# Kernel optimization log

Measured on AMD Instinct MI355X. Metric: run time of the kernel, lower is better.

## Reference

```python
import jax, jax.numpy as jnp
import numpy as np

B, T, N = 256, 4096, 8   # batch, timesteps, n_actions (state channels = 2n)
H = 64                    # hidden width of the t -> latent_x surrogate MLP
P = 2 * N + 2 * N * N     # params dim: g(n) | mu(n) | Pi(n^2) | Gamma(n^2) = 144
DATA_W, PHYS_W, SUP_W = 1.0, 1.0, 1.0


def setup_inputs() -> dict:
    key = jax.random.key(0)
    ks = jax.random.split(key, 10)
    return {
        "t": jax.random.uniform(ks[0], (B, T), dtype=jnp.float32),
        "x_target": jax.random.normal(ks[1], (B, 2 * N, T), dtype=jnp.float32),
        "params_pred": jax.random.normal(ks[2], (B, P), dtype=jnp.float32) * 0.1,
        "params_target": jax.random.normal(ks[3], (B, P), dtype=jnp.float32) * 0.1,
        "ic_pred": jax.random.normal(ks[4], (B, 2 * N), dtype=jnp.float32),
        "ic_target": jax.random.normal(ks[5], (B, 2 * N), dtype=jnp.float32),
        "W1": jax.random.normal(ks[6], (1, H), dtype=jnp.float32) * 0.5,
        "b1": jax.random.normal(ks[7], (H,), dtype=jnp.float32) * 0.1,
        "W2": jax.random.normal(ks[8], (H, 2 * N), dtype=jnp.float32) * 0.2,
        "b2": jax.random.normal(ks[9], (2 * N,), dtype=jnp.float32) * 0.1,
    }


def _observables(latent, mu, n):
    # compute_observables_torch (assumed): obs = [a, relu(q - mu)], smooth=False
    a = latent[..., :n]
    q = latent[..., n:]
    return jnp.concatenate([a, jax.nn.relu(q - mu)], axis=-1)  # (B,T,2n)


def _rhs(state_T, g, mu, Pi, Gamma, n):
    # preference_dynamics_rhs_torch (assumed):
    #   da/dt = g + Pi @ x - a ;  dx/dt = (Gamma @ a) * (mu - x)
    a = state_T[..., :n]            # (B,T,n)
    x = state_T[..., n:]            # (B,T,n)
    da = g + jnp.einsum('bij,btj->bti', Pi, x) - a
    dx = jnp.einsum('bij,btj->bti', Gamma, a) * (mu - x)
    return jnp.concatenate([da, dx], axis=-1)  # (B,T,2n)


def reference(t, x_target, params_pred, params_target, ic_pred, ic_target, W1, b1, W2, b2):
    n = N
    g = params_pred[:, :n]                                    # (B,n)
    mu = params_pred[:, n:2 * n]                              # (B,n)
    Pi = params_pred[:, 2 * n:2 * n + n * n].reshape(B, n, n)
    Gamma = params_pred[:, 2 * n + n * n:].reshape(B, n, n)
    mu_t = mu[:, None, :]                                     # broadcast over T

    def state_fn(tt):
        # surrogate for the upstream net producing latent_x from t (pointwise in t)
        h = jnp.tanh(tt[..., None] @ W1 + b1)   # (B,T,H)
        latent = h @ W2 + b2                    # (B,T,2n)
        return _observables(latent, mu_t, n)    # (B,T,2n)

    # batched d(state)/dt in ONE forward-mode pass (replaces the T-iteration
    # torch.autograd.grad loop); valid because state[b,τ] depends only on t[b,τ].
    state_T, dstate_dt = jax.jvp(state_fn, (t,), (jnp.ones_like(t),))

    state = jnp.transpose(state_T, (0, 2, 1))                 # (B,2n,T)
    data_loss = jnp.mean((state - x_target) ** 2)

    rhs = _rhs(state_T, g[:, None, :], mu_t, Pi, Gamma, n)
    physics_loss = jnp.mean((dstate_dt - rhs) ** 2)

    pred_pi = jnp.concatenate([params_pred, ic_pred], axis=1)
    tgt_pi = jnp.concatenate([params_target, ic_target], axis=1)
    supervised_loss = jnp.mean((pred_pi - tgt_pi) ** 2)

    return DATA_W * data_loss + PHYS_W * physics_loss + SUP_W * supervised_loss
```

## Files before the change

### kernel.cpp

```cpp
#include <hip/hip_runtime.h>
#include <math.h>

#define B_    256
#define T_    4096
#define N_    8
#define TWON_ 16
#define H_    64
#define P_    144
#define BLK   256
#define CHUNKS (T_ / BLK)
#define PSTRIDE 20

#define INV_MAIN  (1.0f / (float)(B_ * TWON_ * T_))
#define INV_SUP   (1.0f / (float)(B_ * (P_ + TWON_)))

#define TWO_LOG2E 2.8853900817779268f

typedef __fp16   half2_t __attribute__((ext_vector_type(2)));
typedef _Float16 half8_t __attribute__((ext_vector_type(8)));
typedef float    f32x4   __attribute__((ext_vector_type(4)));

union HPack { half2_t h2[4]; half8_t h8; };
union RPack { uint4 u4[4]; half2_t h2[16]; };

__device__ __forceinline__ float wave_reduce(float v) {
    #pragma unroll
    for (int off = 32; off > 0; off >>= 1) v += __shfl_down(v, off, 64);
    return v;
}

__global__ __launch_bounds__(BLK)
void pinn_main_kernel(const float* __restrict__ t_in,
                      const float* __restrict__ x_target,
                      const float* __restrict__ params_pred,
                      const float* __restrict__ params_target,
                      const float* __restrict__ ic_pred,
                      const float* __restrict__ ic_target,
                      const float* __restrict__ W1,
                      const float* __restrict__ b1,
                      const float* __restrict__ W2,
                      const float* __restrict__ b2,
                      float* __restrict__ out) {
    __shared__ __align__(16) half2_t spk[BLK * PSTRIDE];
    __shared__ float sg[N_], smu[N_], sPi[N_ * N_], sGam[N_ * N_];
    __shared__ float swsum[BLK / 64];

    const int tid  = threadIdx.x;
    const int b    = blockIdx.y;
    const int lane = tid & 63;
    const int wv   = tid >> 6;
    const int q    = lane >> 4;
    const int mn   = lane & 15;
    const int k0   = q * 8;

    const float* pp = params_pred + b * P_;
    if (tid < N_) { sg[tid] = pp[tid]; smu[tid] = pp[N_ + tid]; }
    if (tid >= 64  && tid < 64 + N_ * N_)  sPi[tid - 64]   = pp[2 * N_ + (tid - 64)];
    if (tid >= 128 && tid < 128 + N_ * N_) sGam[tid - 128] = pp[2 * N_ + N_ * N_ + (tid - 128)];

    float sup = 0.0f;
    if (blockIdx.x == 0) {
        if (tid < P_) {
            const float d = pp[tid] - params_target[b * P_ + tid];
            sup = d * d;
        }
        if (tid < TWON_) {
            const float d = ic_pred[b * TWON_ + tid] - ic_target[b * TWON_ + tid];
            sup = fmaf(d, d, sup);
        }
    }

    float zwlo[8], zblo[8], zwhi[8], zbhi[8];
    HPack Blo, Bhi, Plo, Phi;
    #pragma unroll
    for (int j2 = 0; j2 < 4; ++j2) {
        const int ka = k0 + 2 * j2, kb = ka + 1;
        const float w1a = W1[ka],      w1b = W1[kb];
        const float w1c = W1[32 + ka], w1d = W1[32 + kb];
        zwlo[2*j2] = TWO_LOG2E * w1a; zwlo[2*j2+1] = TWO_LOG2E * w1b;
        zwhi[2*j2] = TWO_LOG2E * w1c; zwhi[2*j2+1] = TWO_LOG2E * w1d;
        zblo[2*j2] = TWO_LOG2E * b1[ka];      zblo[2*j2+1] = TWO_LOG2E * b1[kb];
        zbhi[2*j2] = TWO_LOG2E * b1[32 + ka]; zbhi[2*j2+1] = TWO_LOG2E * b1[32 + kb];
        const float wa = W2[ka * TWON_ + mn],        wb = W2[kb * TWON_ + mn];
        const float wc = W2[(32 + ka) * TWON_ + mn], wd = W2[(32 + kb) * TWON_ + mn];
        Blo.h2[j2] = __builtin_amdgcn_cvt_pkrtz(wa, wb);
        Bhi.h2[j2] = __builtin_amdgcn_cvt_pkrtz(wc, wd);
        Plo.h2[j2] = __builtin_amdgcn_cvt_pkrtz(w1a * wa, w1b * wb);
        Phi.h2[j2] = __builtin_amdgcn_cvt_pkrtz(w1c * wc, w1d * wd);
    }
    const float b2n = b2[mn];

    const float treg = t_in[b * T_ + blockIdx.x * BLK + wv * 64 + lane];

    #pragma unroll
    for (int ti = 0; ti < 4; ++ti) {
        const float tt = __shfl(treg, ti * 16 + mn, 64);

        HPack Ah_lo, Ag_lo, Ah_hi, Ag_hi;
        #pragma unroll
        for (int j2 = 0; j2 < 4; ++j2) {
            float e0 = __builtin_amdgcn_exp2f(fmaf(tt, zwlo[2*j2],   zblo[2*j2]));
            float e1 = __builtin_amdgcn_exp2f(fmaf(tt, zwlo[2*j2+1], zblo[2*j2+1]));
            float r0 = __builtin_amdgcn_rcpf(e0 + 1.0f);
            float r1 = __builtin_amdgcn_rcpf(e1 + 1.0f);
            float h0 = fmaf(-2.0f, r0, 1.0f), h1 = fmaf(-2.0f, r1, 1.0f);
            float g0 = fmaf(-h0, h0, 1.0f),   g1 = fmaf(-h1, h1, 1.0f);
            Ah_lo.h2[j2] = __builtin_amdgcn_cvt_pkrtz(h0, h1);
            Ag_lo.h2[j2] = __builtin_amdgcn_cvt_pkrtz(g0, g1);
            e0 = __builtin_amdgcn_exp2f(fmaf(tt, zwhi[2*j2],   zbhi[2*j2]));
            e1 = __builtin_amdgcn_exp2f(fmaf(tt, zwhi[2*j2+1], zbhi[2*j2+1]));
            r0 = __builtin_amdgcn_rcpf(e0 + 1.0f);
            r1 = __builtin_amdgcn_rcpf(e1 + 1.0f);
            h0 = fmaf(-2.0f, r0, 1.0f); h1 = fmaf(-2.0f, r1, 1.0f);
            g0 = fmaf(-h0, h0, 1.0f);   g1 = fmaf(-h1, h1, 1.0f);
            Ah_hi.h2[j2] = __builtin_amdgcn_cvt_pkrtz(h0, h1);
            Ag_hi.h2[j2] = __builtin_amdgcn_cvt_pkrtz(g0, g1);
        }

        f32x4 lat = {b2n, b2n, b2n, b2n};
        lat = __builtin_amdgcn_mfma_f32_16x16x32_f16(Ah_lo.h8, Blo.h8, lat, 0, 0, 0);
        lat = __builtin_amdgcn_mfma_f32_16x16x32_f16(Ah_hi.h8, Bhi.h8, lat, 0, 0, 0);
        f32x4 dl = {0.0f, 0.0f, 0.0f, 0.0f};
        dl = __builtin_amdgcn_mfma_f32_16x16x32_f16(Ag_lo.h8, Plo.h8, dl, 0, 0, 0);
        dl = __builtin_amdgcn_mfma_f32_16x16x32_f16(Ag_hi.h8, Phi.h8, dl, 0, 0, 0);

        const int rowbase = wv * 64 + ti * 16 + 4 * q;
        #pragma unroll
        for (int r = 0; r < 4; ++r) {
            spk[(rowbase + r) * PSTRIDE + mn] = __builtin_amdgcn_cvt_pkrtz(lat[r], dl[r]);
        }
    }
    __syncthreads();

    float lat[TWON_], dlat[TWON_];
    {
        RPack rp;
        const uint4* pr = (const uint4*)&spk[tid * PSTRIDE];
        #pragma unroll
        for (int c = 0; c < 4; ++c) rp.u4[c] = pr[c];
        #pragma unroll
        for (int i = 0; i < TWON_; ++i) { lat[i] = (float)rp.h2[i].x; dlat[i] = (float)rp.h2[i].y; }
    }

    float a[N_], xs[N_], da_[N_], dxs[N_];
    #pragma unroll
    for (int i = 0; i < N_; ++i) { a[i] = lat[i]; da_[i] = dlat[i]; }
    #pragma unroll
    for (int i = 0; i < N_; ++i) {
        const float qm = lat[N_ + i] - smu[i];
        xs[i]  = qm > 0.0f ? qm : 0.0f;
        dxs[i] = qm > 0.0f ? dlat[N_ + i] : 0.0f;
    }

    float acc = 0.0f;
    const int tq = blockIdx.x * BLK + tid;
    const float* xt = x_target + (size_t)b * TWON_ * T_ + tq;
    #pragma unroll
    for (int k = 0; k < N_; ++k) { const float d = a[k]  - xt[(size_t)k * T_];        acc = fmaf(d, d, acc); }
    #pragma unroll
    for (int k = 0; k < N_; ++k) { const float d = xs[k] - xt[(size_t)(N_ + k) * T_]; acc = fmaf(d, d, acc); }

    #pragma unroll
    for (int i = 0; i < N_; ++i) {
        float s1 = sg[i] - a[i];
        #pragma unroll
        for (int j = 0; j < N_; ++j) s1 = fmaf(sPi[i * N_ + j], xs[j], s1);
        float d = da_[i] - s1;
        acc = fmaf(d, d, acc);

        float s2 = 0.0f;
        #pragma unroll
        for (int j = 0; j < N_; ++j) s2 = fmaf(sGam[i * N_ + j], a[j], s2);
        s2 *= (smu[i] - xs[i]);
        d = dxs[i] - s2;
        acc = fmaf(d, d, acc);
    }

    float v = fmaf(acc, INV_MAIN, sup * INV_SUP);
    float w = wave_reduce(v);
    if ((tid & 63) == 0) swsum[tid >> 6] = w;
    __syncthreads();
    if (tid == 0) {
        float s = 0.0f;
        #pragma unroll
        for (int i = 0; i < BLK / 64; ++i) s += swsum[i];
        atomicAdd(out, s);
    }
}

extern "C" void kernel_launch(void* const* d_in, const int* in_sizes, int n_in,
                              void* d_out, int out_size, void* d_ws, size_t ws_size,
                              hipStream_t stream) {
    const float* t_in          = (const float*)d_in[0];
    const float* x_target      = (const float*)d_in[1];
    const float* params_pred   = (const float*)d_in[2];
    const float* params_target = (const float*)d_in[3];
    const float* ic_pred       = (const float*)d_in[4];
    const float* ic_target     = (const float*)d_in[5];
    const float* W1            = (const float*)d_in[6];
    const float* b1            = (const float*)d_in[7];
    const float* W2            = (const float*)d_in[8];
    const float* b2            = (const float*)d_in[9];
    float* out = (float*)d_out;

    (void)hipMemsetAsync(out, 0, sizeof(float), stream);
    dim3 grid(CHUNKS, B_);
    pinn_main_kernel<<<grid, BLK, 0, stream>>>(t_in, x_target, params_pred,
                                               params_target, ic_pred, ic_target,
                                               W1, b1, W2, b2, out);
}
```

Measured before the change: 157.8 us.

## Use single-wave blocks with workspace partials and a finalize kernel

Shrinks each block to one 64-lane wave, so the grid grows to 64x256 blocks, each writing one partial sum to workspace. A separate single-block finalize kernel reduces all partials, replacing the memset and the global atomicAdd. The x_target loads are hoisted to kernel start so they overlap the MFMA work, and the per-batch parameters are read straight from global/scalar memory instead of shared memory. This removes block-level barriers and atomic contention, at the cost of an extra kernel launch and many more small blocks.

```diff
diff --git a/kernel.cpp b/kernel.cpp
--- a/kernel.cpp
+++ b/kernel.cpp
@@ -7,9 +7,11 @@
 #define TWON_ 16
 #define H_    64
 #define P_    144
-#define BLK   256
-#define CHUNKS (T_ / BLK)
+#define WBLK  64
+#define NBLKX (T_ / WBLK)
+#define NPART (NBLKX * B_)
 #define PSTRIDE 20
+#define FBLK  1024
 
 #define INV_MAIN  (1.0f / (float)(B_ * TWON_ * T_))
 #define INV_SUP   (1.0f / (float)(B_ * (P_ + TWON_)))
@@ -29,7 +31,7 @@
     return v;
 }
 
-__global__ __launch_bounds__(BLK)
+__global__ __launch_bounds__(WBLK, 5)
 void pinn_main_kernel(const float* __restrict__ t_in,
                       const float* __restrict__ x_target,
                       const float* __restrict__ params_pred,
@@ -40,32 +42,32 @@
                       const float* __restrict__ b1,
                       const float* __restrict__ W2,
                       const float* __restrict__ b2,
-                      float* __restrict__ out) {
-    __shared__ __align__(16) half2_t spk[BLK * PSTRIDE];
-    __shared__ float sg[N_], smu[N_], sPi[N_ * N_], sGam[N_ * N_];
-    __shared__ float swsum[BLK / 64];
-
-    const int tid  = threadIdx.x;
+                      float* __restrict__ partials) {
+    __shared__ __align__(16) half2_t spk[WBLK * PSTRIDE];
+
+    const int lane = threadIdx.x;
     const int b    = blockIdx.y;
-    const int lane = tid & 63;
-    const int wv   = tid >> 6;
     const int q    = lane >> 4;
     const int mn   = lane & 15;
     const int k0   = q * 8;
 
     const float* pp = params_pred + b * P_;
-    if (tid < N_) { sg[tid] = pp[tid]; smu[tid] = pp[N_ + tid]; }
-    if (tid >= 64  && tid < 64 + N_ * N_)  sPi[tid - 64]   = pp[2 * N_ + (tid - 64)];
-    if (tid >= 128 && tid < 128 + N_ * N_) sGam[tid - 128] = pp[2 * N_ + N_ * N_ + (tid - 128)];
+
+    const int tq = blockIdx.x * WBLK + lane;
+    const float* xt = x_target + (size_t)b * TWON_ * T_ + tq;
+    float xtv[TWON_];
+    #pragma unroll
+    for (int k = 0; k < TWON_; ++k) xtv[k] = xt[(size_t)k * T_];
 
     float sup = 0.0f;
     if (blockIdx.x == 0) {
-        if (tid < P_) {
-            const float d = pp[tid] - params_target[b * P_ + tid];
-            sup = d * d;
-        }
-        if (tid < TWON_) {
-            const float d = ic_pred[b * TWON_ + tid] - ic_target[b * TWON_ + tid];
+        #pragma unroll
+        for (int i = lane; i < P_; i += WBLK) {
+            const float d = pp[i] - params_target[b * P_ + i];
+            sup = fmaf(d, d, sup);
+        }
+        if (lane < TWON_) {
+            const float d = ic_pred[b * TWON_ + lane] - ic_target[b * TWON_ + lane];
             sup = fmaf(d, d, sup);
         }
     }
@@ -90,7 +92,7 @@
     }
     const float b2n = b2[mn];
 
-    const float treg = t_in[b * T_ + blockIdx.x * BLK + wv * 64 + lane];
+    const float treg = t_in[b * T_ + tq];
 
     #pragma unroll
     for (int ti = 0; ti < 4; ++ti) {
@@ -124,7 +126,7 @@
         dl = __builtin_amdgcn_mfma_f32_16x16x32_f16(Ag_lo.h8, Plo.h8, dl, 0, 0, 0);
         dl = __builtin_amdgcn_mfma_f32_16x16x32_f16(Ag_hi.h8, Phi.h8, dl, 0, 0, 0);
 
-        const int rowbase = wv * 64 + ti * 16 + 4 * q;
+        const int rowbase = ti * 16 + 4 * q;
         #pragma unroll
         for (int r = 0; r < 4; ++r) {
             spk[(rowbase + r) * PSTRIDE + mn] = __builtin_amdgcn_cvt_pkrtz(lat[r], dl[r]);
@@ -135,7 +137,7 @@
     float lat[TWON_], dlat[TWON_];
     {
         RPack rp;
-        const uint4* pr = (const uint4*)&spk[tid * PSTRIDE];
+        const uint4* pr = (const uint4*)&spk[lane * PSTRIDE];
         #pragma unroll
         for (int c = 0; c < 4; ++c) rp.u4[c] = pr[c];
         #pragma unroll
@@ -147,44 +149,62 @@
     for (int i = 0; i < N_; ++i) { a[i] = lat[i]; da_[i] = dlat[i]; }
     #pragma unroll
     for (int i = 0; i < N_; ++i) {
-        const float qm = lat[N_ + i] - smu[i];
+        const float qm = lat[N_ + i] - pp[N_ + i];
         xs[i]  = qm > 0.0f ? qm : 0.0f;
         dxs[i] = qm > 0.0f ? dlat[N_ + i] : 0.0f;
     }
 
     float acc = 0.0f;
-    const int tq = blockIdx.x * BLK + tid;
-    const float* xt = x_target + (size_t)b * TWON_ * T_ + tq;
-    #pragma unroll
-    for (int k = 0; k < N_; ++k) { const float d = a[k]  - xt[(size_t)k * T_];        acc = fmaf(d, d, acc); }
-    #pragma unroll
-    for (int k = 0; k < N_; ++k) { const float d = xs[k] - xt[(size_t)(N_ + k) * T_]; acc = fmaf(d, d, acc); }
-
+    #pragma unroll
+    for (int k = 0; k < N_; ++k) { const float d = a[k]  - xtv[k];      acc = fmaf(d, d, acc); }
+    #pragma unroll
+    for (int k = 0; k < N_; ++k) { const float d = xs[k] - xtv[N_ + k]; acc = fmaf(d, d, acc); }
+
+    const float* Pi  = pp + 2 * N_;
+    const float* Gam = pp + 2 * N_ + N_ * N_;
     #pragma unroll
     for (int i = 0; i < N_; ++i) {
-        float s1 = sg[i] - a[i];
-        #pragma unroll
-        for (int j = 0; j < N_; ++j) s1 = fmaf(sPi[i * N_ + j], xs[j], s1);
+        float s1 = pp[i] - a[i];
+        #pragma unroll
+        for (int j = 0; j < N_; ++j) s1 = fmaf(Pi[i * N_ + j], xs[j], s1);
         float d = da_[i] - s1;
         acc = fmaf(d, d, acc);
 
         float s2 = 0.0f;
         #pragma unroll
-        for (int j = 0; j < N_; ++j) s2 = fmaf(sGam[i * N_ + j], a[j], s2);
-        s2 *= (smu[i] - xs[i]);
+        for (int j = 0; j < N_; ++j) s2 = fmaf(Gam[i * N_ + j], a[j], s2);
+        s2 *= (pp[N_ + i] - xs[i]);
         d = dxs[i] - s2;
         acc = fmaf(d, d, acc);
     }
 
     float v = fmaf(acc, INV_MAIN, sup * INV_SUP);
+    float w = wave_reduce(v);
+    if (lane == 0) partials[blockIdx.y * gridDim.x + blockIdx.x] = w;
+}
+
+__global__ __launch_bounds__(FBLK)
+void pinn_finalize_kernel(const float* __restrict__ partials,
+                          float* __restrict__ out) {
+    __shared__ float swsum[FBLK / 64];
+    const int tid = threadIdx.x;
+
+    const float4* p4 = (const float4*)partials;
+    float v = 0.0f;
+    #pragma unroll
+    for (int c = 0; c < 4; ++c) {
+        const float4 v4 = p4[tid + c * FBLK];
+        v += (v4.x + v4.y) + (v4.z + v4.w);
+    }
+
     float w = wave_reduce(v);
     if ((tid & 63) == 0) swsum[tid >> 6] = w;
     __syncthreads();
     if (tid == 0) {
         float s = 0.0f;
         #pragma unroll
-        for (int i = 0; i < BLK / 64; ++i) s += swsum[i];
-        atomicAdd(out, s);
+        for (int i = 0; i < FBLK / 64; ++i) s += swsum[i];
+        out[0] = s;
     }
 }
 
@@ -202,10 +222,11 @@
     const float* W2            = (const float*)d_in[8];
     const float* b2            = (const float*)d_in[9];
     float* out = (float*)d_out;
-
-    (void)hipMemsetAsync(out, 0, sizeof(float), stream);
-    dim3 grid(CHUNKS, B_);
-    pinn_main_kernel<<<grid, BLK, 0, stream>>>(t_in, x_target, params_pred,
-                                               params_target, ic_pred, ic_target,
-                                               W1, b1, W2, b2, out);
-}
+    float* partials = (float*)d_ws;
+
+    dim3 grid(NBLKX, B_);
+    pinn_main_kernel<<<grid, WBLK, 0, stream>>>(t_in, x_target, params_pred,
+                                                params_target, ic_pred, ic_target,
+                                                W1, b1, W2, b2, partials);
+    pinn_finalize_kernel<<<1, FBLK, 0, stream>>>(partials, out);
+}
```

Result: faster. 130.8 us (-17.1%).
